# Performance work log

Hardware: AMD Instinct MI355X
Metric: run time of the kernel (lower is better)

The kernel has to match this reference:

```python
import jax, jax.numpy as jnp
import numpy as np

K = 512  # number of activations kept per row (init_kwargs k)


def setup_inputs() -> dict:
    key = jax.random.key(0)
    x = jax.random.normal(key, (8192, 8192), dtype=jnp.float32)
    return {"x": x}


def reference(x):
    # torch.topk(x, k, dim=1) -> indices of k largest per row
    _, idx = jax.lax.top_k(x, K)                      # idx: [B, K]
    rows = jnp.arange(x.shape[0])[:, None]            # [B, 1]
    # zeros_like + scatter(1, idx, 1)
    mask = jnp.zeros_like(x).at[rows, idx].set(1.0)   # [B, F]
    return x * mask
```

## Files before the change

### kernel.cpp

```cpp
#include <hip/hip_runtime.h>
#include <stdint.h>

#define FDIM 8192
#define KSEL 512
#define NT   512
#define EPT  (FDIM / NT / 4)
#define NBIN 4096
#define NWAVE (NT / 64)
#define NBLK 1024
#define RPB  (FDIM / NBLK)

__device__ __forceinline__ unsigned keyOf(unsigned u) {
    return u ^ ((unsigned)((int)u >> 31) | 0x80000000u);
}
__device__ __forceinline__ float valOf(unsigned key) {
    unsigned u = (key & 0x80000000u) ? (key ^ 0x80000000u) : ~key;
    return __uint_as_float(u);
}

__device__ __forceinline__ void barrier_lgkm() {
    asm volatile("s_waitcnt lgkmcnt(0)" ::: "memory");
    __builtin_amdgcn_s_barrier();
}
__device__ __forceinline__ void barrier_full() {
    asm volatile("s_waitcnt vmcnt(0) lgkmcnt(0)" ::: "memory");
    __builtin_amdgcn_s_barrier();
}

struct Shared {
    uint4 hist4[NBIN / 4];
    unsigned wtot[NWAVE];
    unsigned s_prefix, s_need;
    unsigned s_thresh, s_keepEq, s_eqCnt;
    unsigned s_tiecnt;
    unsigned tiebuf[64];
};

__device__ __forceinline__ void process_row(
    const int row, const bool doPrefetch, const int nextRow,
    const float* __restrict__ x, float* __restrict__ out,
    uint4 (&cur)[EPT], uint4 (&nxt)[EPT],
    Shared& sh, const int t, const int lane, const int wave)
{
    if (doPrefetch) {
        const uint4* xr = (const uint4*)(x + (size_t)nextRow * FDIM);
        #pragma unroll
        for (int j = 0; j < EPT; ++j) nxt[j] = xr[j * NT + t];
    }

    #pragma unroll
    for (int j = 0; j < EPT; ++j) {
        cur[j].x = keyOf(cur[j].x);
        cur[j].y = keyOf(cur[j].y);
        cur[j].z = keyOf(cur[j].z);
        cur[j].w = keyOf(cur[j].w);
    }
    if (t == 0) { sh.s_prefix = 0u; sh.s_need = KSEL; sh.s_tiecnt = 0u; }
    barrier_lgkm();

    unsigned* hist = (unsigned*)sh.hist4;

    #pragma unroll
    for (int round = 0; round < 3; ++round) {
        const unsigned pref = sh.s_prefix;
        const unsigned need = sh.s_need;

        if (round == 0) {
            #pragma unroll
            for (int j = 0; j < EPT; ++j) {
                #pragma unroll
                for (int c = 0; c < 4; ++c) {
                    unsigned key = (&cur[j].x)[c];
                    atomicAdd(&hist[key >> 20], 1u);
                }
            }
        } else if (round == 1) {
            #pragma unroll
            for (int j = 0; j < EPT; ++j) {
                #pragma unroll
                for (int c = 0; c < 4; ++c) {
                    unsigned key = (&cur[j].x)[c];
                    if ((key >> 20) == pref)
                        atomicAdd(&hist[(key >> 8) & 0xFFFu], 1u);
                }
            }
        } else {
            #pragma unroll
            for (int j = 0; j < EPT; ++j) {
                #pragma unroll
                for (int c = 0; c < 4; ++c) {
                    unsigned key = (&cur[j].x)[c];
                    if ((key >> 8) == pref)
                        atomicAdd(&hist[key & 0xFFu], 1u);
                }
            }
        }
        barrier_lgkm();

        const unsigned b4 = (unsigned)t * 2u;
        const uint4 h0 = sh.hist4[b4];
        const uint4 h1 = sh.hist4[b4 + 1];
        unsigned sfx[9];
        sfx[8] = 0u;
        sfx[7] = h1.w;
        sfx[6] = sfx[7] + h1.z;
        sfx[5] = sfx[6] + h1.y;
        sfx[4] = sfx[5] + h1.x;
        sfx[3] = sfx[4] + h0.w;
        sfx[2] = sfx[3] + h0.z;
        sfx[1] = sfx[2] + h0.y;
        sfx[0] = sfx[1] + h0.x;
        sh.hist4[b4]     = make_uint4(0u, 0u, 0u, 0u);
        sh.hist4[b4 + 1] = make_uint4(0u, 0u, 0u, 0u);
        const unsigned tot = sfx[0];
        unsigned incl = tot;
        #pragma unroll
        for (int off = 1; off < 64; off <<= 1) {
            unsigned y = __shfl_down(incl, off);
            incl += (lane + off < 64) ? y : 0u;
        }
        if (lane == 0) sh.wtot[wave] = incl;
        barrier_lgkm();

        unsigned gb = incl - tot;
        #pragma unroll
        for (int w = 0; w < NWAVE; ++w) gb += (w > wave) ? sh.wtot[w] : 0u;

        const unsigned base = (unsigned)t * (NBIN / NT);
        #pragma unroll
        for (int i = 0; i < 8; ++i) {
            unsigned S = gb + sfx[i];
            unsigned h = sfx[i] - sfx[i + 1];
            if (S >= need && S - h < need) {
                if (round == 2) {
                    sh.s_thresh = (pref << 8) | (base + (unsigned)i);
                    sh.s_keepEq = need - (S - h);
                    sh.s_eqCnt  = h;
                } else {
                    sh.s_prefix = (pref << 12) | (base + (unsigned)i);
                    sh.s_need   = need - (S - h);
                }
            }
        }
        barrier_lgkm();
    }

    const unsigned thresh = sh.s_thresh;
    const unsigned keepEq = sh.s_keepEq;
    const unsigned eqCnt  = sh.s_eqCnt;
    const bool simple = (eqCnt == keepEq);

    float4* orow = (float4*)(out + (size_t)row * FDIM);

    if (simple) {
        #pragma unroll
        for (int j = 0; j < EPT; ++j) {
            uint4 k = cur[j];
            float4 o;
            o.x = (k.x >= thresh) ? valOf(k.x) : 0.0f;
            o.y = (k.y >= thresh) ? valOf(k.y) : 0.0f;
            o.z = (k.z >= thresh) ? valOf(k.z) : 0.0f;
            o.w = (k.w >= thresh) ? valOf(k.w) : 0.0f;
            orow[j * NT + t] = o;
        }
    } else {
        #pragma unroll
        for (int j = 0; j < EPT; ++j) {
            uint4 k = cur[j];
            float4 o;
            o.x = (k.x > thresh) ? valOf(k.x) : 0.0f;
            o.y = (k.y > thresh) ? valOf(k.y) : 0.0f;
            o.z = (k.z > thresh) ? valOf(k.z) : 0.0f;
            o.w = (k.w > thresh) ? valOf(k.w) : 0.0f;
            orow[j * NT + t] = o;
        }
        #pragma unroll
        for (int j = 0; j < EPT; ++j) {
            #pragma unroll
            for (int c = 0; c < 4; ++c) {
                unsigned key = (&cur[j].x)[c];
                if (key == thresh) {
                    unsigned slot = atomicAdd(&sh.s_tiecnt, 1u);
                    if (slot < 64u) sh.tiebuf[slot] = 4u * (unsigned)(j * NT + t) + (unsigned)c;
                }
            }
        }
        barrier_full();
        if (t == 0) {
            const unsigned m = sh.s_tiecnt;
            const float v = valOf(thresh);
            if (m <= 64u) {
                for (unsigned i = 0; i < m; ++i) {
                    unsigned idx = sh.tiebuf[i], rank = 0;
                    for (unsigned q = 0; q < m; ++q) rank += (sh.tiebuf[q] < idx);
                    if (rank < keepEq) out[(size_t)row * FDIM + idx] = v;
                }
            } else {
                unsigned c = 0;
                for (int i = 0; i < FDIM && c < keepEq; ++i) {
                    if (keyOf(__float_as_uint(x[(size_t)row * FDIM + i])) == thresh) {
                        out[(size_t)row * FDIM + i] = v; ++c;
                    }
                }
            }
        }
    }
}

__global__ __launch_bounds__(NT, 4) void topk_mask_kernel(const float* __restrict__ x,
                                                          float* __restrict__ out) {
    __shared__ Shared sh;

    const int blk  = blockIdx.x;
    const int t    = threadIdx.x;
    const int lane = t & 63;
    const int wave = t >> 6;

    uint4 rawA[EPT], rawB[EPT];
    {
        const uint4* xr = (const uint4*)(x + (size_t)blk * FDIM);
        #pragma unroll
        for (int j = 0; j < EPT; ++j) rawA[j] = xr[j * NT + t];
    }
    #pragma unroll
    for (int i = t; i < NBIN / 4; i += NT) sh.hist4[i] = make_uint4(0u, 0u, 0u, 0u);

    #pragma unroll 1
    for (int r = 0; r < RPB; r += 2) {
        process_row(r * NBLK + blk, true, (r + 1) * NBLK + blk,
                    x, out, rawA, rawB, sh, t, lane, wave);
        process_row((r + 1) * NBLK + blk, (r + 2) < RPB, (r + 2) * NBLK + blk,
                    x, out, rawB, rawA, sh, t, lane, wave);
    }
}

extern "C" void kernel_launch(void* const* d_in, const int* in_sizes, int n_in,
                              void* d_out, int out_size, void* d_ws, size_t ws_size,
                              hipStream_t stream) {
    const float* x = (const float*)d_in[0];
    float* out = (float*)d_out;
    topk_mask_kernel<<<dim3(NBLK), dim3(NT), 0, stream>>>(x, out);
}
```

Baseline: 444.8 us.

## Shrink radix histogram to 2048 bins with sign-split first pass

Replaces the 4096-bin 12/12/8 radix select with an 11-bit first pass split by sign, followed by two 10-bit passes, so the shared histogram drops to 8 KB. The first pass counts only positive keys and falls back to negative keys only when fewer than K positives exist, which removes most of the atomics for typical data. Launch bounds are raised to 8 blocks per CU to use the smaller LDS footprint, at the cost of tighter register limits and possible spills given the two 16-element prefetch buffers. The fallback adds an extra histogram pass and scan on rows that need it.

```diff
diff --git a/kernel.cpp b/kernel.cpp
--- a/kernel.cpp
+++ b/kernel.cpp
@@ -5,13 +5,13 @@
 #define KSEL 512
 #define NT   512
 #define EPT  (FDIM / NT / 4)
-#define NBIN 4096
+#define NBINP 2048
 #define NWAVE (NT / 64)
 #define NBLK 1024
 #define RPB  (FDIM / NBLK)
 
 __device__ __forceinline__ unsigned keyOf(unsigned u) {
-    return u ^ ((unsigned)((int)u >> 31) | 0x80000000u);
+    return (u & 0x80000000u) ? ~u : (u | 0x80000000u);
 }
 __device__ __forceinline__ float valOf(unsigned key) {
     unsigned u = (key & 0x80000000u) ? (key ^ 0x80000000u) : ~key;
@@ -27,8 +27,8 @@
     __builtin_amdgcn_s_barrier();
 }
 
-struct Shared {
-    uint4 hist4[NBIN / 4];
+struct SharedT {
+    uint4 hist4[NBINP / 4];
     unsigned wtot[NWAVE];
     unsigned s_prefix, s_need;
     unsigned s_thresh, s_keepEq, s_eqCnt;
@@ -40,48 +40,103 @@
     const int row, const bool doPrefetch, const int nextRow,
     const float* __restrict__ x, float* __restrict__ out,
     uint4 (&cur)[EPT], uint4 (&nxt)[EPT],
-    Shared& sh, const int t, const int lane, const int wave)
+    SharedT& sh, const int t, const int lane, const int wave)
 {
+    unsigned* hist  = (unsigned*)sh.hist4;
+    uint2*    hist2 = (uint2*)sh.hist4;
+
     if (doPrefetch) {
         const uint4* xr = (const uint4*)(x + (size_t)nextRow * FDIM);
         #pragma unroll
         for (int j = 0; j < EPT; ++j) nxt[j] = xr[j * NT + t];
     }
-
-    #pragma unroll
-    for (int j = 0; j < EPT; ++j) {
-        cur[j].x = keyOf(cur[j].x);
-        cur[j].y = keyOf(cur[j].y);
-        cur[j].z = keyOf(cur[j].z);
-        cur[j].w = keyOf(cur[j].w);
-    }
-    if (t == 0) { sh.s_prefix = 0u; sh.s_need = KSEL; sh.s_tiecnt = 0u; }
-    barrier_lgkm();
-
-    unsigned* hist = (unsigned*)sh.hist4;
-
-    #pragma unroll
-    for (int round = 0; round < 3; ++round) {
-        const unsigned pref = sh.s_prefix;
-        const unsigned need = sh.s_need;
-
-        if (round == 0) {
+    if (t == 0) sh.s_tiecnt = 0u;
+
+    auto scan2048 = [&](unsigned needP, unsigned prefOr) -> unsigned {
+        const uint4 h0 = sh.hist4[t];
+        unsigned sfx[5];
+        sfx[4] = 0u;
+        sfx[3] = h0.w;
+        sfx[2] = sfx[3] + h0.z;
+        sfx[1] = sfx[2] + h0.y;
+        sfx[0] = sfx[1] + h0.x;
+        sh.hist4[t] = make_uint4(0u, 0u, 0u, 0u);
+        const unsigned tot = sfx[0];
+        unsigned incl = tot;
+        #pragma unroll
+        for (int off = 1; off < 64; off <<= 1) {
+            unsigned y = __shfl_down(incl, off);
+            incl += (lane + off < 64) ? y : 0u;
+        }
+        if (lane == 0) sh.wtot[wave] = incl;
+        barrier_lgkm();
+        unsigned gb = incl - tot, grand = 0u;
+        #pragma unroll
+        for (int w = 0; w < NWAVE; ++w) {
+            grand += sh.wtot[w];
+            gb += (w > wave) ? sh.wtot[w] : 0u;
+        }
+        const unsigned base = (unsigned)t * 4u;
+        #pragma unroll
+        for (int i = 0; i < 4; ++i) {
+            unsigned S = gb + sfx[i];
+            unsigned h = sfx[i] - sfx[i + 1];
+            if (S >= needP && S - h < needP) {
+                sh.s_prefix = prefOr | (base + (unsigned)i);
+                sh.s_need   = needP - (S - h);
+            }
+        }
+        return grand;
+    };
+
+    {
+        unsigned need = KSEL;
+        #pragma unroll
+        for (int j = 0; j < EPT; ++j) {
+            cur[j].x = keyOf(cur[j].x);
+            cur[j].y = keyOf(cur[j].y);
+            cur[j].z = keyOf(cur[j].z);
+            cur[j].w = keyOf(cur[j].w);
+            #pragma unroll
+            for (int c = 0; c < 4; ++c) {
+                unsigned key = (&cur[j].x)[c];
+                if (key & 0x80000000u)
+                    atomicAdd(&hist[(key >> 20) & 0x7FFu], 1u);
+            }
+        }
+        barrier_lgkm();
+        unsigned grand = scan2048(need, 0x800u);
+        barrier_lgkm();
+        if (grand < need) {
+            need -= grand;
             #pragma unroll
             for (int j = 0; j < EPT; ++j) {
                 #pragma unroll
                 for (int c = 0; c < 4; ++c) {
                     unsigned key = (&cur[j].x)[c];
-                    atomicAdd(&hist[key >> 20], 1u);
-                }
-            }
-        } else if (round == 1) {
+                    if (!(key & 0x80000000u))
+                        atomicAdd(&hist[key >> 20], 1u);
+                }
+            }
+            barrier_lgkm();
+            (void)scan2048(need, 0u);
+            barrier_lgkm();
+        }
+    }
+
+    #pragma unroll
+    for (int round = 1; round < 3; ++round) {
+        const unsigned pref = sh.s_prefix;
+        const unsigned need = sh.s_need;
+
+        if (round == 1) {
             #pragma unroll
             for (int j = 0; j < EPT; ++j) {
                 #pragma unroll
                 for (int c = 0; c < 4; ++c) {
                     unsigned key = (&cur[j].x)[c];
                     if ((key >> 20) == pref)
-                        atomicAdd(&hist[(key >> 8) & 0xFFFu], 1u);
+                        atomicAdd(&hist[(key >> 10) & 0x3FFu], 1u);
                 }
             }
         } else {
@@ -90,28 +145,19 @@
                 #pragma unroll
                 for (int c = 0; c < 4; ++c) {
                     unsigned key = (&cur[j].x)[c];
-                    if ((key >> 8) == pref)
-                        atomicAdd(&hist[key & 0xFFu], 1u);
-                }
-            }
-        }
-        barrier_lgkm();
-
-        const unsigned b4 = (unsigned)t * 2u;
-        const uint4 h0 = sh.hist4[b4];
-        const uint4 h1 = sh.hist4[b4 + 1];
-        unsigned sfx[9];
-        sfx[8] = 0u;
-        sfx[7] = h1.w;
-        sfx[6] = sfx[7] + h1.z;
-        sfx[5] = sfx[6] + h1.y;
-        sfx[4] = sfx[5] + h1.x;
-        sfx[3] = sfx[4] + h0.w;
-        sfx[2] = sfx[3] + h0.z;
-        sfx[1] = sfx[2] + h0.y;
-        sfx[0] = sfx[1] + h0.x;
-        sh.hist4[b4]     = make_uint4(0u, 0u, 0u, 0u);
-        sh.hist4[b4 + 1] = make_uint4(0u, 0u, 0u, 0u);
+                    if ((key >> 10) == pref)
+                        atomicAdd(&hist[key & 0x3FFu], 1u);
+                }
+            }
+        }
+        barrier_lgkm();
+
+        const uint2 h = hist2[t];
+        unsigned sfx[3];
+        sfx[2] = 0u;
+        sfx[1] = h.y;
+        sfx[0] = h.y + h.x;
+        hist2[t] = make_uint2(0u, 0u);
         const unsigned tot = sfx[0];
         unsigned incl = tot;
         #pragma unroll
@@ -121,24 +167,23 @@
         }
         if (lane == 0) sh.wtot[wave] = incl;
         barrier_lgkm();
-
         unsigned gb = incl - tot;
         #pragma unroll
         for (int w = 0; w < NWAVE; ++w) gb += (w > wave) ? sh.wtot[w] : 0u;
 
-        const unsigned base = (unsigned)t * (NBIN / NT);
-        #pragma unroll
-        for (int i = 0; i < 8; ++i) {
+        const unsigned base = (unsigned)t * 2u;
+        #pragma unroll
+        for (int i = 0; i < 2; ++i) {
             unsigned S = gb + sfx[i];
-            unsigned h = sfx[i] - sfx[i + 1];
-            if (S >= need && S - h < need) {
+            unsigned h2 = sfx[i] - sfx[i + 1];
+            if (S >= need && S - h2 < need) {
                 if (round == 2) {
-                    sh.s_thresh = (pref << 8) | (base + (unsigned)i);
-                    sh.s_keepEq = need - (S - h);
-                    sh.s_eqCnt  = h;
+                    sh.s_thresh = (pref << 10) | (base + (unsigned)i);
+                    sh.s_keepEq = need - (S - h2);
+                    sh.s_eqCnt  = h2;
                 } else {
-                    sh.s_prefix = (pref << 12) | (base + (unsigned)i);
-                    sh.s_need   = need - (S - h);
+                    sh.s_prefix = (pref << 10) | (base + (unsigned)i);
+                    sh.s_need   = need - (S - h2);
                 }
             }
         }
@@ -207,9 +252,9 @@
     }
 }
 
-__global__ __launch_bounds__(NT, 4) void topk_mask_kernel(const float* __restrict__ x,
+__global__ __launch_bounds__(NT, 8) void topk_mask_kernel(const float* __restrict__ x,
                                                           float* __restrict__ out) {
-    __shared__ Shared sh;
+    __shared__ SharedT sh;
 
     const int blk  = blockIdx.x;
     const int t    = threadIdx.x;
@@ -222,14 +267,15 @@
         #pragma unroll
         for (int j = 0; j < EPT; ++j) rawA[j] = xr[j * NT + t];
     }
-    #pragma unroll
-    for (int i = t; i < NBIN / 4; i += NT) sh.hist4[i] = make_uint4(0u, 0u, 0u, 0u);
+    sh.hist4[t] = make_uint4(0u, 0u, 0u, 0u);
+    barrier_lgkm();
 
     #pragma unroll 1
     for (int r = 0; r < RPB; r += 2) {
         process_row(r * NBLK + blk, true, (r + 1) * NBLK + blk,
                     x, out, rawA, rawB, sh, t, lane, wave);
-        process_row((r + 1) * NBLK + blk, (r + 2) < RPB, (r + 2) * NBLK + blk,
+        process_row((r + 1) * NBLK + blk, (r + 2) < RPB,
+                    ((r + 2) < RPB ? (r + 2) : 0) * NBLK + blk,
                     x, out, rawB, rawA, sh, t, lane, wave);
     }
 }
```

After: 462.5 us. 1.04x slower.
